# Performance work log

Measured on AMD Instinct MI355X. Metric: run time of the kernel, lower is better.

Reference implementation:

```python
import jax, jax.numpy as jnp
import numpy as np

NUM_SLOTS = 3
NUM_ORIENTS = 8
PATCH_SIZE = 81  # 9x9 board
BUY_SIZE = NUM_SLOTS * NUM_ORIENTS * PATCH_SIZE  # 1944
ACTIONS = 1 + PATCH_SIZE + BUY_SIZE  # 2026
NEG = -1.0e9
EPS = 1e-5

B = 4096
C_IN = 256
HID = 256


def setup_inputs() -> dict:
    key = jax.random.key(0)
    ks = jax.random.split(key, 12)
    s = 0.05
    return {
        "x": jax.random.normal(ks[0], (B, C_IN, 9, 9), jnp.float32),
        "action_mask": jax.random.randint(ks[1], (B, ACTIONS), 0, 2, dtype=jnp.int32),
        # p_conv: 1x1 conv, no bias (use_batch_norm=True) -> weight (HID, C_IN)
        "conv_w": jax.random.normal(ks[2], (HID, C_IN), jnp.float32) * s,
        # BatchNorm2d (inference form with running stats)
        "bn_gamma": jnp.ones((HID,), jnp.float32),
        "bn_beta": jnp.zeros((HID,), jnp.float32),
        "bn_mean": jax.random.normal(ks[3], (HID,), jnp.float32) * 0.1,
        "bn_var": jax.random.uniform(ks[4], (HID,), jnp.float32, 0.5, 1.5),
        "type_w": jax.random.normal(ks[5], (3, HID), jnp.float32) * s,
        "type_b": jnp.zeros((3,), jnp.float32),
        "patch_w": jax.random.normal(ks[6], (1, HID), jnp.float32) * s,
        "patch_b": jnp.zeros((1,), jnp.float32),
        "slot_w": jax.random.normal(ks[7], (NUM_SLOTS, HID), jnp.float32) * s,
        "slot_b": jnp.zeros((NUM_SLOTS,), jnp.float32),
        "orient_w": jax.random.normal(ks[8], (NUM_SLOTS * NUM_ORIENTS, HID), jnp.float32) * s,
        "orient_b": jnp.zeros((NUM_SLOTS * NUM_ORIENTS,), jnp.float32),
        "pos_w": jax.random.normal(ks[9], (NUM_SLOTS * NUM_ORIENTS, HID), jnp.float32) * s,
        "pos_b": jnp.zeros((NUM_SLOTS * NUM_ORIENTS,), jnp.float32),
    }


def _masked_logsoftmax(logits, mask_bool):
    lg = jnp.where(mask_bool, logits, NEG)
    return jnp.maximum(jax.nn.log_softmax(lg, axis=-1), -100.0)


def reference(x, action_mask, conv_w, bn_gamma, bn_beta, bn_mean, bn_var,
              type_w, type_b, patch_w, patch_b, slot_w, slot_b,
              orient_w, orient_b, pos_w, pos_b):
    b = x.shape[0]
    # 1x1 conv + BN (eval) + ReLU
    p = jnp.einsum('bchw,oc->bohw', x, conv_w)
    scale = bn_gamma * jax.lax.rsqrt(bn_var + EPS)
    p = jax.nn.relu(p * scale[None, :, None, None] + (bn_beta - bn_mean * scale)[None, :, None, None])
    p_mean = p.mean(axis=(2, 3))  # (B, HID)

    # masks from action_mask layout [pass | 81 patch | 1944 buy]
    am = action_mask > 0
    patch_mask = am[:, 1:1 + PATCH_SIZE]
    buy4d = am[:, 82:82 + BUY_SIZE].reshape(b, NUM_SLOTS, NUM_ORIENTS, PATCH_SIZE)
    type_mask = jnp.stack([am[:, 0], patch_mask.any(-1), buy4d.reshape(b, -1).any(-1)], axis=-1)
    orient_mask = buy4d.any(-1)
    slot_mask = orient_mask.any(-1)

    type_lp = _masked_logsoftmax(p_mean @ type_w.T + type_b, type_mask)          # (B,3)
    patch_logits = jnp.einsum('bchw,oc->bohw', p, patch_w).reshape(b, PATCH_SIZE) \
        + patch_b[0]
    patch_lp = _masked_logsoftmax(patch_logits, patch_mask)                       # (B,81)
    slot_lp = _masked_logsoftmax(p_mean @ slot_w.T + slot_b, slot_mask)           # (B,3)
    orient_lp = _masked_logsoftmax(
        (p_mean @ orient_w.T + orient_b).reshape(b, NUM_SLOTS, NUM_ORIENTS), orient_mask)
    pos_logits = (jnp.einsum('bchw,oc->bohw', p, pos_w) + pos_b[None, :, None, None]) \
        .reshape(b, NUM_SLOTS, NUM_ORIENTS, PATCH_SIZE)
    pos_lp = _masked_logsoftmax(pos_logits, buy4d)                                # (B,3,8,81)

    pass_lp = type_lp[:, 0:1]
    patch_joint = type_lp[:, 1:2] + patch_lp
    buy_joint = (type_lp[:, 2:3, None, None] + slot_lp[:, :, None, None]
                 + orient_lp[:, :, :, None] + pos_lp).reshape(b, BUY_SIZE)
    return jnp.concatenate([pass_lp, patch_joint, buy_joint], axis=1)  # (B, 2026)
```

## Files before the change

kernel.cpp:

```cpp
#include <hip/hip_runtime.h>

#define ACT 2026
#define NEGV -1.0e9f

typedef short short8 __attribute__((ext_vector_type(8)));
typedef float f32x4 __attribute__((ext_vector_type(4)));

__device__ __forceinline__ unsigned f2bf(float f) {
  unsigned u = __float_as_uint(f);
  return (u + 0x7FFFu + ((u >> 16) & 1u)) >> 16;
}

__device__ __forceinline__ unsigned cvtpk(float lo, float hi) {
  unsigned r;
  asm("v_cvt_pk_bf16_f32 %0, %1, %2" : "=v"(r) : "v"(lo), "v"(hi));
  return r;
}

#define GL16(gp, lp) __builtin_amdgcn_global_load_lds(                         \
    (const __attribute__((address_space(1))) void*)(gp),                       \
    (__attribute__((address_space(3))) void*)(lp), 16, 0, 0)

__global__ void prep_w_kernel(const float* __restrict__ conv_w,
                              const float* __restrict__ pos_w,
                              const float* __restrict__ patch_w,
                              unsigned short* __restrict__ wimg,
                              unsigned short* __restrict__ w2img) {
  int g = blockIdx.x * 256 + threadIdx.x;
  if (g < 8192) {
    int r = g & 15, gq = (g >> 4) & 3, mtg = (g >> 6) & 15, ks = g >> 10;
    const float* src = conv_w + (mtg * 16 + r) * 256 + ks * 32 + gq * 8;
    unsigned v0 = f2bf(src[0]) | (f2bf(src[1]) << 16);
    unsigned v1 = f2bf(src[2]) | (f2bf(src[3]) << 16);
    unsigned v2 = f2bf(src[4]) | (f2bf(src[5]) << 16);
    unsigned v3 = f2bf(src[6]) | (f2bf(src[7]) << 16);
    uint4 q; q.x = v0; q.y = v1; q.z = v2; q.w = v3;
    *(uint4*)(wimg + g * 8) = q;
  } else if (g < 9216) {
    int g2 = g - 8192;
    int r = g2 & 15, gq = (g2 >> 4) & 3, mt = (g2 >> 6) & 1, ks2 = g2 >> 7;
    int m2 = mt * 16 + r;
    int o0 = ks2 * 32 + gq * 8;
    unsigned short v[8];
#pragma unroll
    for (int e = 0; e < 8; ++e) {
      float f = 0.f;
      if (m2 < 24) f = pos_w[m2 * 256 + o0 + e];
      else if (m2 == 24) f = patch_w[o0 + e];
      v[e] = (unsigned short)f2bf(f);
    }
    uint4 q;
    q.x = (unsigned)v[0] | ((unsigned)v[1] << 16);
    q.y = (unsigned)v[2] | ((unsigned)v[3] << 16);
    q.z = (unsigned)v[4] | ((unsigned)v[5] << 16);
    q.w = (unsigned)v[6] | ((unsigned)v[7] << 16);
    *(uint4*)(w2img + g2 * 8) = q;
  }
}

__global__ __launch_bounds__(256, 3)
void policy_main(const float* __restrict__ x,
                 const int* __restrict__ am,
                 const unsigned short* __restrict__ wimg,
                 const unsigned short* __restrict__ w2img,
                 const float* __restrict__ bn_gamma, const float* __restrict__ bn_beta,
                 const float* __restrict__ bn_mean, const float* __restrict__ bn_var,
                 const float* __restrict__ type_w, const float* __restrict__ type_b,
                 const float* __restrict__ patch_b,
                 const float* __restrict__ slot_w, const float* __restrict__ slot_b,
                 const float* __restrict__ orient_w, const float* __restrict__ orient_b,
                 const float* __restrict__ pos_b,
                 float* __restrict__ out)
{
  __shared__ __align__(16) char s_big[49152];
  __shared__ __align__(16) float s_scale[256];
  __shared__ __align__(16) float s_bias[256];
  __shared__ __align__(16) float s_pmean[256];
  __shared__ float s_part[240];
  __shared__ float s_hl[30];
  __shared__ float s_tlp[3], s_slp[3], s_olp[24];
  __shared__ int s_omask[24];
  __shared__ int s_misc[6];

  char* xband = s_big;
  unsigned short* pT = (unsigned short*)s_big;
  float* s_out2 = (float*)s_big;

  const int tid = threadIdx.x;
  const int w  = tid >> 6;
  const int l  = tid & 63;
  const int b  = blockIdx.x;
  const float* xb = x + (size_t)b * (256 * 81);

  {
    float sc = bn_gamma[tid] * rsqrtf(bn_var[tid] + 1e-5f);
    s_scale[tid] = sc;
    s_bias[tid]  = bn_beta[tid] - bn_mean[tid] * sc;
  }

  const int kg = l >> 4;
  const int kr = l & 15;
  const int g4 = kg * 4;

  f32x4 acc[4][6];
#pragma unroll
  for (int i = 0; i < 4; ++i)
#pragma unroll
    for (int j = 0; j < 6; ++j) {
      f32x4 z = {0.f, 0.f, 0.f, 0.f};
      acc[i][j] = z;
    }

  auto STAGE = [&](int ks) {
    const char* g = (const char*)xb + ks * 10368;
    char* lb = xband + (ks & 1) * 10368;
    GL16(g + tid * 16,         lb + w * 1024);
    GL16(g + (256 + tid) * 16, lb + 4096 + w * 1024);
    if (tid < 136)   GL16(g + (512 + tid) * 16, lb + 8192 + w * 1024);
    else if (w == 3) GL16(g + (576 + l) * 16,   lb + 9216);
  };

  auto LDA = [&](int ks, short8 (&d)[4]) {
    const unsigned short* ab = wimg + ks * 8192 + w * 2048 + kg * 128 + kr * 8;
    d[0] = *(const short8*)(ab);
    d[1] = *(const short8*)(ab + 512);
    d[2] = *(const short8*)(ab + 1024);
    d[3] = *(const short8*)(ab + 1536);
  };

  short8 afA[4], afB[4];
  LDA(0, afA);
  STAGE(0);
  __syncthreads();

  auto STEP = [&](int k, short8 (&cur)[4], short8 (&nxt)[4]) {
    if (k < 7) {
      STAGE(k + 1);
      LDA(k + 1, nxt);
    }
    const float* xt = (const float*)(xband + (k & 1) * 10368);
    const float* colb = xt + kg * 648 + kr;
#pragma unroll
    for (int nt = 0; nt < 6; ++nt) {
      const float* col = colb + nt * 16;
      float f0 = col[0],   f1 = col[81],  f2 = col[162], f3 = col[243];
      float f4 = col[324], f5 = col[405], f6 = col[486], f7 = col[567];
      union { unsigned u[4]; short8 s; } bf;
      bf.u[0] = cvtpk(f0, f1);
      bf.u[1] = cvtpk(f2, f3);
      bf.u[2] = cvtpk(f4, f5);
      bf.u[3] = cvtpk(f6, f7);
      acc[0][nt] = __builtin_amdgcn_mfma_f32_16x16x32_bf16(cur[0], bf.s, acc[0][nt], 0, 0, 0);
      acc[1][nt] = __builtin_amdgcn_mfma_f32_16x16x32_bf16(cur[1], bf.s, acc[1][nt], 0, 0, 0);
      acc[2][nt] = __builtin_amdgcn_mfma_f32_16x16x32_bf16(cur[2], bf.s, acc[2][nt], 0, 0, 0);
      acc[3][nt] = __builtin_amdgcn_mfma_f32_16x16x32_bf16(cur[3], bf.s, acc[3][nt], 0, 0, 0);
    }
    __syncthreads();
  };

  STEP(0, afA, afB);
  STEP(1, afB, afA);
  STEP(2, afA, afB);
  STEP(3, afB, afA);
  STEP(4, afA, afB);
  STEP(5, afB, afA);
  STEP(6, afA, afB);
  STEP(7, afB, afA);

#pragma unroll
  for (int mi = 0; mi < 4; ++mi) {
    int ob = w * 64 + mi * 16 + g4;
    float sc0 = s_scale[ob], sc1 = s_scale[ob + 1], sc2 = s_scale[ob + 2], sc3 = s_scale[ob + 3];
    float bi0 = s_bias[ob],  bi1 = s_bias[ob + 1],  bi2 = s_bias[ob + 2],  bi3 = s_bias[ob + 3];
    float vs0 = 0.f, vs1 = 0.f, vs2 = 0.f, vs3 = 0.f;
    int ks2 = ob >> 5;
    int j2  = (ob >> 3) & 3;
    int e0  = ob & 7;
    char* pbase = (char*)pT + ks2 * 6144 + j2 * 256 + kr * 16 + e0 * 2;
#pragma unroll
    for (int nt = 0; nt < 6; ++nt) {
      float v0 = fmaxf(acc[mi][nt][0] * sc0 + bi0, 0.f);
      float v1 = fmaxf(acc[mi][nt][1] * sc1 + bi1, 0.f);
      float v2 = fmaxf(acc[mi][nt][2] * sc2 + bi2, 0.f);
      float v3 = fmaxf(acc[mi][nt][3] * sc3 + bi3, 0.f);
      if (nt < 5 || kr == 0) { vs0 += v0; vs1 += v1; vs2 += v2; vs3 += v3; }
      uint2 pvv;
      pvv.x = cvtpk(v0, v1);
      pvv.y = cvtpk(v2, v3);
      *(uint2*)(pbase + nt * 1024) = pvv;
    }
    float vv[4] = {vs0, vs1, vs2, vs3};
#pragma unroll
    for (int i = 0; i < 4; ++i) {
      float s = vv[i];
      s += __shfl_xor(s, 1);
      s += __shfl_xor(s, 2);
      s += __shfl_xor(s, 4);
      s += __shfl_xor(s, 8);
      vv[i] = s;
    }
    if (kr == 0) {
      s_pmean[ob]     = vv[0] * (1.f / 81.f);
      s_pmean[ob + 1] = vv[1] * (1.f / 81.f);
      s_pmean[ob + 2] = vv[2] * (1.f / 81.f);
      s_pmean[ob + 3] = vv[3] * (1.f / 81.f);
    }
  }

  const int* amr = am + (size_t)b * ACT;
  for (int t = w; t < 25; t += 4) {
    int off = (t < 24) ? (82 + t * 81) : 1;
    int v1 = amr[off + l];
    int v2 = (l < 17) ? amr[off + 64 + l] : 0;
    unsigned long long bal = __ballot((v1 | v2) != 0);
    if (l == 0) {
      int any = (bal != 0ULL) ? 1 : 0;
      if (t < 24) s_omask[t] = any; else s_misc[0] = any;
    }
  }
  __syncthreads();

  {
    const int mt  = w & 1;
    const int ntb = (w >> 1) * 3;
    f32x4 acc2[3];
#pragma unroll
    for (int t = 0; t < 3; ++t) { f32x4 z = {0.f, 0.f, 0.f, 0.f}; acc2[t] = z; }
#pragma unroll
    for (int ks2 = 0; ks2 < 8; ++ks2) {
      const unsigned short* ap = w2img + ((ks2 * 2 + mt) * 4 + kg) * 128 + kr * 8;
      short8 a2 = *(const short8*)ap;
#pragma unroll
      for (int t = 0; t < 3; ++t) {
        const short8* bp = (const short8*)((const char*)pT + ks2 * 6144 + (ntb + t) * 1024 + kg * 256 + kr * 16);
        acc2[t] = __builtin_amdgcn_mfma_f32_16x16x32_bf16(a2, *bp, acc2[t], 0, 0, 0);
      }
    }
    __syncthreads();
#pragma unroll
    for (int t = 0; t < 3; ++t) {
      int hw = (ntb + t) * 16 + kr;
      int m2 = mt * 16 + g4;
#pragma unroll
      for (int i = 0; i < 4; ++i)
        s_out2[(m2 + i) * 104 + hw] = acc2[t][i];
    }
  }

  if (tid < 240) {
    int h = tid >> 3, seg = tid & 7;
    const float* wp = (h < 3) ? (type_w + h * 256)
                    : (h < 6) ? (slot_w + (h - 3) * 256)
                              : (orient_w + (h - 6) * 256);
    float p = 0.f;
    int base = seg * 32;
#pragma unroll 8
    for (int e = 0; e < 32; ++e) p += s_pmean[base + e] * wp[base + e];
    s_part[tid] = p;
  }
  __syncthreads();

  if (tid < 30) {
    float a = 0.f;
#pragma unroll
    for (int e = 0; e < 8; ++e) a += s_part[tid * 8 + e];
    a += (tid < 3) ? type_b[tid] : (tid < 6) ? slot_b[tid - 3] : orient_b[tid - 6];
    s_hl[tid] = a;
  }
  if (tid == 32) {
    int sa0 = 0, sa1 = 0, sa2 = 0;
#pragma unroll
    for (int r = 0; r < 8; ++r) { sa0 |= s_omask[r]; sa1 |= s_omask[8 + r]; sa2 |= s_omask[16 + r]; }
    s_misc[1] = sa0; s_misc[2] = sa1; s_misc[3] = sa2;
    s_misc[4] = sa0 | sa1 | sa2;
  }
  __syncthreads();

  if (tid == 0) {
    int mk0 = amr[0] > 0, mk1 = s_misc[0], mk2 = s_misc[4];
    float g0 = mk0 ? s_hl[0] : NEGV;
    float g1 = mk1 ? s_hl[1] : NEGV;
    float g2 = mk2 ? s_hl[2] : NEGV;
    float m = fmaxf(fmaxf(g0, g1), g2);
    float sum = __expf(g0 - m) + __expf(g1 - m) + __expf(g2 - m);
    float ls = m + __logf(sum);
    s_tlp[0] = fmaxf(g0 - ls, -100.f);
    s_tlp[1] = fmaxf(g1 - ls, -100.f);
    s_tlp[2] = fmaxf(g2 - ls, -100.f);
  } else if (tid == 1) {
    float g[3]; float m = -3.0e38f;
#pragma unroll
    for (int s = 0; s < 3; ++s) { g[s] = s_misc[1 + s] ? s_hl[3 + s] : NEGV; m = fmaxf(m, g[s]); }
    float sum = 0.f;
#pragma unroll
    for (int s = 0; s < 3; ++s) sum += __expf(g[s] - m);
    float ls = m + __logf(sum);
#pragma unroll
    for (int s = 0; s < 3; ++s) s_slp[s] = fmaxf(g[s] - ls, -100.f);
  } else if (tid >= 2 && tid < 5) {
    int s = tid - 2;
    float g[8]; float m = -3.0e38f;
#pragma unroll
    for (int r = 0; r < 8; ++r) { g[r] = s_omask[s * 8 + r] ? s_hl[6 + s * 8 + r] : NEGV; m = fmaxf(m, g[r]); }
    float sum = 0.f;
#pragma unroll
    for (int r = 0; r < 8; ++r) sum += __expf(g[r] - m);
    float ls = m + __logf(sum);
#pragma unroll
    for (int r = 0; r < 8; ++r) s_olp[s * 8 + r] = fmaxf(g[r] - ls, -100.f);
  }
  __syncthreads();

  float* ob_out = out + (size_t)b * ACT;
  for (int t = w; t < 25; t += 4) {
    int off = (t < 24) ? (82 + t * 81) : 1;
    float badd = (t < 24) ? pos_b[t] : patch_b[0];
    int a1 = amr[off + l];
    int a2v = (l < 17) ? amr[off + 64 + l] : 0;
    float lg1 = (a1 > 0) ? (s_out2[t * 104 + l] + badd) : NEGV;
    float lg2 = (l < 17 && a2v > 0) ? (s_out2[t * 104 + 64 + l] + badd) : NEGV;
    float mx = fmaxf(lg1, (l < 17) ? lg2 : -3.0e38f);
#pragma unroll
    for (int mm = 1; mm < 64; mm <<= 1) mx = fmaxf(mx, __shfl_xor(mx, mm));
    float sm = __expf(lg1 - mx) + ((l < 17) ? __expf(lg2 - mx) : 0.f);
#pragma unroll
    for (int mm = 1; mm < 64; mm <<= 1) sm += __shfl_xor(sm, mm);
    float lse = mx + __logf(sm);
    float lp1 = fmaxf(lg1 - lse, -100.f);
    float lp2 = fmaxf(lg2 - lse, -100.f);
    float addj; int obase;
    if (t < 24) { addj = s_tlp[2] + s_slp[t >> 3] + s_olp[t]; obase = 82 + t * 81; }
    else        { addj = s_tlp[1];                             obase = 1; }
    ob_out[obase + l] = addj + lp1;
    if (l < 17) ob_out[obase + 64 + l] = addj + lp2;
    if (t == 24 && l == 0) ob_out[0] = s_tlp[0];
  }
}

extern "C" void kernel_launch(void* const* d_in, const int* in_sizes, int n_in,
                              void* d_out, int out_size, void* d_ws, size_t ws_size,
                              hipStream_t stream) {
  (void)in_sizes; (void)n_in; (void)out_size; (void)ws_size;
  const float* x        = (const float*)d_in[0];
  const int*   amask    = (const int*)d_in[1];
  const float* conv_w   = (const float*)d_in[2];
  const float* bn_gamma = (const float*)d_in[3];
  const float* bn_beta  = (const float*)d_in[4];
  const float* bn_mean  = (const float*)d_in[5];
  const float* bn_var   = (const float*)d_in[6];
  const float* type_w   = (const float*)d_in[7];
  const float* type_b   = (const float*)d_in[8];
  const float* patch_w  = (const float*)d_in[9];
  const float* patch_b  = (const float*)d_in[10];
  const float* slot_w   = (const float*)d_in[11];
  const float* slot_b   = (const float*)d_in[12];
  const float* orient_w = (const float*)d_in[13];
  const float* orient_b = (const float*)d_in[14];
  const float* pos_w    = (const float*)d_in[15];
  const float* pos_b    = (const float*)d_in[16];
  float* outp = (float*)d_out;

  unsigned short* wimg  = (unsigned short*)d_ws;
  unsigned short* w2img = wimg + 65536;

  prep_w_kernel<<<36, 256, 0, stream>>>(conv_w, pos_w, patch_w, wimg, w2img);
  policy_main<<<4096, 256, 0, stream>>>(x, amask, wimg, w2img,
                                        bn_gamma, bn_beta, bn_mean, bn_var,
                                        type_w, type_b, patch_b,
                                        slot_w, slot_b, orient_w, orient_b,
                                        pos_b, outp);
}
```

Measured before the change: 209.3 us.

## Convert x tile to bf16 once per block in a shared LDS image

Before, each of the four waves read the same fp32 x tile from LDS and converted it to bf16 on its own, which repeated the LDS reads and conversions four times. Now the block cooperatively transposes and packs each k-slice into a double-buffered bf16 fragment image in LDS. Each wave then loads ready-made short8 B fragments. The pipeline is reorganised so that stage k+2 loads, k+1 is transposed, and k is multiplied in the same step. In exchange, the weight fragments are no longer prefetched a step ahead, so their global load latency is exposed inside each step.

```diff
diff --git a/kernel.cpp b/kernel.cpp
--- a/kernel.cpp
+++ b/kernel.cpp
@@ -82,7 +82,8 @@
   __shared__ int s_omask[24];
   __shared__ int s_misc[6];
 
-  char* xband = s_big;
+  char* f32buf = s_big;
+  char* bfimg  = s_big + 20736;
   unsigned short* pT = (unsigned short*)s_big;
   float* s_out2 = (float*)s_big;
 
@@ -113,59 +114,73 @@
 
   auto STAGE = [&](int ks) {
     const char* g = (const char*)xb + ks * 10368;
-    char* lb = xband + (ks & 1) * 10368;
+    char* lb = f32buf + (ks & 1) * 10368;
     GL16(g + tid * 16,         lb + w * 1024);
     GL16(g + (256 + tid) * 16, lb + 4096 + w * 1024);
     if (tid < 136)   GL16(g + (512 + tid) * 16, lb + 8192 + w * 1024);
     else if (w == 3) GL16(g + (576 + l) * 16,   lb + 9216);
   };
 
-  auto LDA = [&](int ks, short8 (&d)[4]) {
-    const unsigned short* ab = wimg + ks * 8192 + w * 2048 + kg * 128 + kr * 8;
-    d[0] = *(const short8*)(ab);
-    d[1] = *(const short8*)(ab + 512);
-    d[2] = *(const short8*)(ab + 1024);
-    d[3] = *(const short8*)(ab + 1536);
+  auto TRANSPOSE = [&](int t) {
+    const float* src = (const float*)(f32buf + (t & 1) * 10368);
+    char* dst = bfimg + (t & 1) * 6144;
+    {
+      int q = tid;
+      int nt_ = q >> 6, kr_ = (q >> 2) & 15, kg_ = q & 3;
+      const float* s = src + kg_ * 648 + nt_ * 16 + kr_;
+      uint4 v;
+      v.x = cvtpk(s[0],   s[81]);
+      v.y = cvtpk(s[162], s[243]);
+      v.z = cvtpk(s[324], s[405]);
+      v.w = cvtpk(s[486], s[567]);
+      *(uint4*)(dst + q * 16) = v;
+    }
+    if (tid < 128) {
+      int q = 256 + tid;
+      int nt_ = q >> 6, kr_ = (q >> 2) & 15, kg_ = q & 3;
+      const float* s = src + kg_ * 648 + nt_ * 16 + kr_;
+      uint4 v;
+      v.x = cvtpk(s[0],   s[81]);
+      v.y = cvtpk(s[162], s[243]);
+      v.z = cvtpk(s[324], s[405]);
+      v.w = cvtpk(s[486], s[567]);
+      *(uint4*)(dst + q * 16) = v;
+    }
   };
 
-  short8 afA[4], afB[4];
-  LDA(0, afA);
   STAGE(0);
-  __syncthreads();
-
-  auto STEP = [&](int k, short8 (&cur)[4], short8 (&nxt)[4]) {
-    if (k < 7) {
-      STAGE(k + 1);
-      LDA(k + 1, nxt);
-    }
-    const float* xt = (const float*)(xband + (k & 1) * 10368);
-    const float* colb = xt + kg * 648 + kr;
+  STAGE(1);
+  __syncthreads();
+  TRANSPOSE(0);
+  __syncthreads();
+
+  const int fragoff = (kr * 4 + kg) * 16;
+
+  auto STEP = [&](int k) {
+    if (k + 2 < 8) STAGE(k + 2);
+    short8 af[4];
+    {
+      const unsigned short* ab = wimg + k * 8192 + w * 2048 + kg * 128 + kr * 8;
+      af[0] = *(const short8*)(ab);
+      af[1] = *(const short8*)(ab + 512);
+      af[2] = *(const short8*)(ab + 1024);
+      af[3] = *(const short8*)(ab + 1536);
+    }
+    if (k + 1 < 8) TRANSPOSE(k + 1);
+    const char* bi = bfimg + (k & 1) * 6144;
 #pragma unroll
     for (int nt = 0; nt < 6; ++nt) {
-      const float* col = colb + nt * 16;
-      float f0 = col[0],   f1 = col[81],  f2 = col[162], f3 = col[243];
-      float f4 = col[324], f5 = col[405], f6 = col[486], f7 = col[567];
-      union { unsigned u[4]; short8 s; } bf;
-      bf.u[0] = cvtpk(f0, f1);
-      bf.u[1] = cvtpk(f2, f3);
-      bf.u[2] = cvtpk(f4, f5);
-      bf.u[3] = cvtpk(f6, f7);
-      acc[0][nt] = __builtin_amdgcn_mfma_f32_16x16x32_bf16(cur[0], bf.s, acc[0][nt], 0, 0, 0);
-      acc[1][nt] = __builtin_amdgcn_mfma_f32_16x16x32_bf16(cur[1], bf.s, acc[1][nt], 0, 0, 0);
-      acc[2][nt] = __builtin_amdgcn_mfma_f32_16x16x32_bf16(cur[2], bf.s, acc[2][nt], 0, 0, 0);
-      acc[3][nt] = __builtin_amdgcn_mfma_f32_16x16x32_bf16(cur[3], bf.s, acc[3][nt], 0, 0, 0);
+      short8 bf = *(const short8*)(bi + nt * 1024 + fragoff);
+      acc[0][nt] = __builtin_amdgcn_mfma_f32_16x16x32_bf16(af[0], bf, acc[0][nt], 0, 0, 0);
+      acc[1][nt] = __builtin_amdgcn_mfma_f32_16x16x32_bf16(af[1], bf, acc[1][nt], 0, 0, 0);
+      acc[2][nt] = __builtin_amdgcn_mfma_f32_16x16x32_bf16(af[2], bf, acc[2][nt], 0, 0, 0);
+      acc[3][nt] = __builtin_amdgcn_mfma_f32_16x16x32_bf16(af[3], bf, acc[3][nt], 0, 0, 0);
     }
     __syncthreads();
   };
 
-  STEP(0, afA, afB);
-  STEP(1, afB, afA);
-  STEP(2, afA, afB);
-  STEP(3, afB, afA);
-  STEP(4, afA, afB);
-  STEP(5, afB, afA);
-  STEP(6, afA, afB);
-  STEP(7, afB, afA);
+  STEP(0); STEP(1); STEP(2); STEP(3);
+  STEP(4); STEP(5); STEP(6); STEP(7);
 
 #pragma unroll
   for (int mi = 0; mi < 4; ++mi) {
```

Result: slower. 216.6 us (+3.5%).
